# Performance work log

Hardware: AMD Instinct MI355X
Metric: run time of the kernel (lower is better)

## Reference

```python
import jax, jax.numpy as jnp
import numpy as np

B, N, DM, H = 2, 512, 1024, 16  # batch, seq, d_model, n_heads
DEPTHS = [1, 2, 4, 8]
LAM = 0.1  # lambda_distance


def setup_inputs() -> dict:
    key = jax.random.key(0)
    ks = jax.random.split(key, 2 + 5 * len(DEPTHS))
    inp = {
        "x": jax.random.normal(ks[0], (B, N, DM), jnp.float32),
        "depth_logits": jax.random.normal(ks[1], (len(DEPTHS),), jnp.float32),
    }
    j = 2
    for i, D in enumerate(DEPTHS):
        ds = DM // D
        r = max(1, D // 4)
        inp[f"pe{i}"] = jax.random.normal(ks[j], (N, D, ds), jnp.float32) * 0.02; j += 1
        inp[f"wqkv{i}"] = jax.random.normal(ks[j], (D, ds, 3 * ds), jnp.float32) / np.sqrt(ds); j += 1
        inp[f"wo{i}"] = jax.random.normal(ks[j], (DM, DM), jnp.float32) / np.sqrt(DM); j += 1
        inp[f"fu{i}"] = jax.random.normal(ks[j], (D, r), jnp.float32) / np.sqrt(r); j += 1
        inp[f"fv{i}"] = jax.random.normal(ks[j], (r, D), jnp.float32); j += 1
    return inp


def _ring_bias(n, lam, dtype):
    # toroidal (circular) distance bias on the sequence ring, normalized by N/2
    idx = jnp.arange(n)
    diff = jnp.abs(idx[:, None] - idx[None, :])
    ring = jnp.minimum(diff, n - diff).astype(dtype)
    return -lam * ring * (2.0 / n)  # [N, N]


def _toroidal_branch(x, pe, wqkv, wo, fu, fv):
    # x: [B, N, DM]; pe: [N, D, ds]; wqkv: [D, ds, 3ds]; wo: [DM, DM]; fu@fv: [D, D]
    b, n, dm = x.shape
    d_depth, ds, _ = wqkv.shape
    hd = ds // H
    xs = x.reshape(b, n, d_depth, ds) + pe[None]          # [B, N, D, ds]
    qkv = jnp.einsum('bnds,dse->bnde', xs, wqkv)          # per-depth-slice projection
    q, k, v = jnp.split(qkv, 3, axis=-1)
    q = q.reshape(b, n, d_depth, H, hd)
    k = k.reshape(b, n, d_depth, H, hd)
    v = v.reshape(b, n, d_depth, H, hd)
    bias = _ring_bias(n, LAM, x.dtype)
    scores = jnp.einsum('bndhe,bmdhe->bdhnm', q, k) / jnp.sqrt(jnp.asarray(hd, x.dtype))
    attn = jax.nn.softmax(scores + bias, axis=-1)          # [B, D, H, N, N]
    o = jnp.einsum('bdhnm,bmdhe->bndhe', attn, v).reshape(b, n, d_depth, ds)
    mix = fu @ fv                                          # low-rank depth fusion [D, D]
    fused = jnp.einsum('df,bnfs->bnds', mix, o).reshape(b, n, dm)
    return fused @ wo


def _forward(x, depth_logits, pe0, wqkv0, wo0, fu0, fv0, pe1, wqkv1, wo1, fu1, fv1,
             pe2, wqkv2, wo2, fu2, fv2, pe3, wqkv3, wo3, fu3, fv3):
    # inference-mode depth selection: hard one-hot at argmax (all branches still computed)
    w = jax.nn.one_hot(jnp.argmax(depth_logits), depth_logits.shape[0], dtype=x.dtype)
    params = [(pe0, wqkv0, wo0, fu0, fv0), (pe1, wqkv1, wo1, fu1, fv1),
              (pe2, wqkv2, wo2, fu2, fv2), (pe3, wqkv3, wo3, fu3, fv3)]
    out = jnp.zeros_like(x)
    for i, p in enumerate(params):
        out = out + w[i] * _toroidal_branch(x, *p)
    return out


def reference(x, depth_logits, pe0, wqkv0, wo0, fu0, fv0, pe1, wqkv1, wo1, fu1, fv1,
              pe2, wqkv2, wo2, fu2, fv2, pe3, wqkv3, wo3, fu3, fv3):
    return _forward(x, depth_logits, pe0, wqkv0, wo0, fu0, fv0, pe1, wqkv1, wo1, fu1, fv1,
                    pe2, wqkv2, wo2, fu2, fv2, pe3, wqkv3, wo3, fu3, fv3)
```

## Files before the change

### kernel.cpp

```cpp
#include <hip/hip_runtime.h>

#define B_   2
#define N_   512
#define DM_  1024
#define H_   16
#define LAM_ 0.1f

typedef __attribute__((ext_vector_type(8))) short bf16x8;
typedef __attribute__((ext_vector_type(4))) float f32x4;
typedef unsigned short ush;
struct ush4 { ush x, y, z, w; };
struct uint2s { unsigned x, y; };

__device__ inline ush f2bf(float v) {
    union { float f; unsigned u; } c; c.f = v;
    unsigned r = c.u + 0x7FFF + ((c.u >> 16) & 1);
    return (ush)(r >> 16);
}
__device__ inline float bf2f(ush b) {
    union { float f; unsigned u; } c; c.u = ((unsigned)b) << 16; return c.f;
}
__device__ inline f32x4 mfma16(bf16x8 a, bf16x8 b, f32x4 c) {
    return __builtin_amdgcn_mfma_f32_16x16x32_bf16(a, b, c, 0, 0, 0);
}

__global__ void k_select(const float* __restrict__ logits, int* __restrict__ sel) {
    if (threadIdx.x == 0) {
        float best = logits[0]; int bi = 0;
        for (int i = 1; i < 4; ++i) { float v = logits[i]; if (v > best) { best = v; bi = i; } }
        *sel = bi;
    }
}

template<int D>
__device__ void prep_wt_tile(int bT, int tid, const float* __restrict__ w,
                             ush* __restrict__ wh, ush* __restrict__ wl,
                             float (*lds)[65]) {
    constexpr int ds = DM_ / D;
    constexpr int tpr = 3 * ds / 64;
    constexpr int tpc = ds / 64;
    constexpr int tpd = tpr * tpc;
    if (bT >= D * tpd) return;
    const int d = bT / tpd, rem = bT % tpd;
    const int tr = rem / tpr, tc = rem % tpr;
    const float* src = w + (size_t)d * ds * 3 * ds;
    ush* dsth = wh + (size_t)d * 3 * ds * ds;
    ush* dstl = wl + (size_t)d * 3 * ds * ds;
    const int c = tid & 63, r0 = tid >> 6;
    #pragma unroll
    for (int j = 0; j < 16; ++j) {
        const int r = j * 4 + r0;
        lds[r][c] = src[(size_t)(tr * 64 + r) * (3 * ds) + tc * 64 + c];
    }
    __syncthreads();
    #pragma unroll
    for (int j = 0; j < 16; ++j) {
        const int r = j * 4 + r0;
        const float v = lds[c][r];
        const size_t o = (size_t)(tc * 64 + r) * ds + tr * 64 + c;
        const ush h = f2bf(v);
        dsth[o] = h; dstl[o] = f2bf(v - bf2f(h));
    }
}
__global__ __launch_bounds__(256) void k_prep(
        const int* __restrict__ sel, const float* __restrict__ x,
        const float* __restrict__ pe0, const float* __restrict__ pe1,
        const float* __restrict__ pe2, const float* __restrict__ pe3,
        const float* __restrict__ w0, const float* __restrict__ w1,
        const float* __restrict__ w2, const float* __restrict__ w3,
        const float* __restrict__ wo0, const float* __restrict__ wo1,
        const float* __restrict__ wo2, const float* __restrict__ wo3,
        ush* __restrict__ xh, ush* __restrict__ xl,
        ush* __restrict__ wqh, ush* __restrict__ wql,
        ush* __restrict__ woh, ush* __restrict__ wol) {
    __shared__ float lds[64][65];
    const int s = *sel;
    const int bid = blockIdx.x, tid = threadIdx.x;
    if (bid < 1024) {
        const float* pe = (s == 0) ? pe0 : (s == 1) ? pe1 : (s == 2) ? pe2 : pe3;
        const size_t i0 = ((size_t)bid * 256 + tid) * 4;
        const float4 xv = *(const float4*)&x[i0];
        const float4 pv = *(const float4*)&pe[i0 & ((size_t)N_ * DM_ - 1)];
        ush4 h4, l4;
        float v;
        v = xv.x + pv.x; h4.x = f2bf(v); l4.x = f2bf(v - bf2f(h4.x));
        v = xv.y + pv.y; h4.y = f2bf(v); l4.y = f2bf(v - bf2f(h4.y));
        v = xv.z + pv.z; h4.z = f2bf(v); l4.z = f2bf(v - bf2f(h4.z));
        v = xv.w + pv.w; h4.w = f2bf(v); l4.w = f2bf(v - bf2f(h4.w));
        *(ush4*)&xh[i0] = h4;
        *(ush4*)&xl[i0] = l4;
    } else if (bid < 1792) {
        const int bT = bid - 1024;
        switch (s) {
            case 0: prep_wt_tile<1>(bT, tid, w0, wqh, wql, lds); break;
            case 1: prep_wt_tile<2>(bT, tid, w1, wqh, wql, lds); break;
            case 2: prep_wt_tile<4>(bT, tid, w2, wqh, wql, lds); break;
            case 3: prep_wt_tile<8>(bT, tid, w3, wqh, wql, lds); break;
        }
    } else {
        const float* w = (s == 0) ? wo0 : (s == 1) ? wo1 : (s == 2) ? wo2 : wo3;
        const int bT = bid - 1792;
        const int tr = bT >> 4, tc = bT & 15;
        const int c = tid & 63, r0 = tid >> 6;
        #pragma unroll
        for (int j = 0; j < 16; ++j) {
            const int r = j * 4 + r0;
            lds[r][c] = w[(size_t)(tr * 64 + r) * DM_ + tc * 64 + c];
        }
        __syncthreads();
        #pragma unroll
        for (int j = 0; j < 16; ++j) {
            const int r = j * 4 + r0;
            const float v = lds[c][r];
            const size_t o = (size_t)(tc * 64 + r) * DM_ + tr * 64 + c;
            const ush h = f2bf(v);
            woh[o] = h; wol[o] = f2bf(v - bf2f(h));
        }
    }
}

template<int KD>
__device__ void gemm_core(const ush* __restrict__ Ah, const ush* __restrict__ Al, int lda,
                          const ush* __restrict__ Bh, const ush* __restrict__ Bl, int ldb,
                          int row0, int col0, int tid, ush* lds, f32x4 acc[2][2]) {
    ush* lAh = lds; ush* lAl = lds + 2560; ush* lBh = lds + 5120; ush* lBl = lds + 7680;
    const int srow = tid >> 2, scg = tid & 3;
    const int lane = tid & 63, w = tid >> 6;
    const int wm = w >> 1, wn = w & 1;
    const int lr = lane & 15, lb = lane >> 4;

    for (int k0 = 0; k0 < KD; k0 += 32) {
        *(bf16x8*)&lAh[srow * 40 + scg * 8] =
            *(const bf16x8*)&Ah[(size_t)(row0 + srow) * lda + k0 + scg * 8];
        *(bf16x8*)&lAl[srow * 40 + scg * 8] =
            *(const bf16x8*)&Al[(size_t)(row0 + srow) * lda + k0 + scg * 8];
        *(bf16x8*)&lBh[srow * 40 + scg * 8] =
            *(const bf16x8*)&Bh[(size_t)(col0 + srow) * ldb + k0 + scg * 8];
        *(bf16x8*)&lBl[srow * 40 + scg * 8] =
            *(const bf16x8*)&Bl[(size_t)(col0 + srow) * ldb + k0 + scg * 8];
        __syncthreads();
        bf16x8 ah[2], al[2], bh[2], bl[2];
        #pragma unroll
        for (int mg = 0; mg < 2; ++mg) {
            const int r = wm * 32 + mg * 16 + lr;
            ah[mg] = *(const bf16x8*)&lAh[r * 40 + lb * 8];
            al[mg] = *(const bf16x8*)&lAl[r * 40 + lb * 8];
        }
        #pragma unroll
        for (int ng = 0; ng < 2; ++ng) {
            const int r = wn * 32 + ng * 16 + lr;
            bh[ng] = *(const bf16x8*)&lBh[r * 40 + lb * 8];
            bl[ng] = *(const bf16x8*)&lBl[r * 40 + lb * 8];
        }
        #pragma unroll
        for (int mg = 0; mg < 2; ++mg)
            #pragma unroll
            for (int ng = 0; ng < 2; ++ng) {
                acc[mg][ng] = mfma16(ah[mg], bh[ng], acc[mg][ng]);
                acc[mg][ng] = mfma16(al[mg], bh[ng], acc[mg][ng]);
                acc[mg][ng] = mfma16(ah[mg], bl[ng], acc[mg][ng]);
            }
        __syncthreads();
    }
}

template<int D>
__device__ void qkv_body(int bid, int tid,
                         const ush* __restrict__ xh, const ush* __restrict__ xl,
                         const ush* __restrict__ wh, const ush* __restrict__ wl,
                         ush* __restrict__ Qh, ush* __restrict__ Ql,
                         ush* __restrict__ Kh, ush* __restrict__ Kl,
                         ush* __restrict__ Vth, ush* __restrict__ Vtl, ush* lds) {
    constexpr int ds = DM_ / D;
    constexpr int hd = ds / H_;
    constexpr int nx = 3 * ds / 64;
    const int bx = bid % nx, by = (bid / nx) & 7, bz = bid / (nx * 8);
    const int b = bz / D, d = bz % D;
    const int row0 = by * 64, col0 = bx * 64;

    f32x4 acc[2][2] = {};
    gemm_core<ds>(xh + (size_t)b * N_ * DM_ + d * ds, xl + (size_t)b * N_ * DM_ + d * ds, DM_,
                  wh + (size_t)d * 3 * ds * ds, wl + (size_t)d * 3 * ds * ds, ds,
                  row0, col0, tid, lds, acc);

    const int lane = tid & 63, w = tid >> 6;
    const int wm = w >> 1, wn = w & 1;
    const int lr = lane & 15, lb = lane >> 4;
    #pragma unroll
    for (int mg = 0; mg < 2; ++mg)
        #pragma unroll
        for (int ng = 0; ng < 2; ++ng) {
            const int n0 = row0 + wm * 32 + mg * 16 + lb * 4;
            const int e  = col0 + wn * 32 + ng * 16 + lr;
            const int part = e / ds, ep = e % ds;
            const int h = ep / hd, t = ep % hd;
            const size_t head = ((size_t)b * D + d) * H_ + h;
            if (part == 2) {
                ush4 h4, l4;
                const float v0 = acc[mg][ng][0], v1 = acc[mg][ng][1];
                const float v2 = acc[mg][ng][2], v3 = acc[mg][ng][3];
                h4.x = f2bf(v0); l4.x = f2bf(v0 - bf2f(h4.x));
                h4.y = f2bf(v1); l4.y = f2bf(v1 - bf2f(h4.y));
                h4.z = f2bf(v2); l4.z = f2bf(v2 - bf2f(h4.z));
                h4.w = f2bf(v3); l4.w = f2bf(v3 - bf2f(h4.w));
                const size_t o = (head * hd + t) * N_ + n0;
                *(ush4*)&Vth[o] = h4;
                *(ush4*)&Vtl[o] = l4;
            } else {
                #pragma unroll
                for (int i = 0; i < 4; ++i) {
                    const size_t o = (head * N_ + n0 + i) * hd + t;
                    const float v = acc[mg][ng][i];
                    const ush hh = f2bf(v), ll = f2bf(v - bf2f(hh));
                    if (part == 0) { Qh[o] = hh; Ql[o] = ll; }
                    else           { Kh[o] = hh; Kl[o] = ll; }
                }
            }
        }
}
__global__ __launch_bounds__(256) void k_qkv(
        const int* __restrict__ sel,
        const ush* __restrict__ xh, const ush* __restrict__ xl,
        const ush* __restrict__ wh, const ush* __restrict__ wl,
        ush* __restrict__ Qh, ush* __restrict__ Ql,
        ush* __restrict__ Kh, ush* __restrict__ Kl,
        ush* __restrict__ Vth, ush* __restrict__ Vtl) {
    __shared__ ush lds[4 * 2560];
    const int bid = blockIdx.x, tid = threadIdx.x;
    switch (*sel) {
        case 0: qkv_body<1>(bid, tid, xh, xl, wh, wl, Qh, Ql, Kh, Kl, Vth, Vtl, lds); break;
        case 1: qkv_body<2>(bid, tid, xh, xl, wh, wl, Qh, Ql, Kh, Kl, Vth, Vtl, lds); break;
        case 2: qkv_body<4>(bid, tid, xh, xl, wh, wl, Qh, Ql, Kh, Kl, Vth, Vtl, lds); break;
        case 3: qkv_body<8>(bid, tid, xh, xl, wh, wl, Qh, Ql, Kh, Kl, Vth, Vtl, lds); break;
    }
}

template<int D>
__device__ void attn_body(int bid, int tid,
        const ush* __restrict__ Qh, const ush* __restrict__ Ql,
        const ush* __restrict__ Kh, const ush* __restrict__ Kl,
        const ush* __restrict__ Vth, const ush* __restrict__ Vtl,
        float* __restrict__ O, ush* P, float* redl) {
    constexpr int ds = DM_ / D, hd = ds / H_;
    constexpr int CH = (hd >= 64) ? 2 : 1;
    constexpr int NT = (hd >= 16) ? hd / 16 : 1;
    constexpr int NHEAD = B_ * D * H_;
    constexpr int NB = NHEAD * 32;
    if (bid >= NB) return;
    const int bidr = (bid & 7) * (NB / 8) + (bid >> 3);
    const int head = bidr >> 5, qt = bidr & 31;
    const int h = head % H_, d = (head / H_) % D, b = head / (H_ * D);
    const int q0 = qt * 16;
    const size_t hb = (size_t)head * N_ * hd;
    const int lane = tid & 63, wk = tid >> 6;
    const int lr = lane & 15, lb = lane >> 4;
    const float L2E = 1.44269504f;
    const float SC  = rsqrtf((float)hd) * L2E;
    const float RB2 = LAM_ * (2.0f / N_) * L2E;
    const bf16x8 z8 = {0, 0, 0, 0, 0, 0, 0, 0};

    bf16x8 qah[CH], qal[CH];
    #pragma unroll
    for (int c = 0; c < CH; ++c) {
        const int k0 = c * 32 + lb * 8;
        bf16x8 vh = z8, vl = z8;
        if (k0 < hd) {
            const size_t o = hb + (size_t)(q0 + lr) * hd + k0;
            vh = *(const bf16x8*)&Qh[o];
            vl = *(const bf16x8*)&Ql[o];
        }
        qah[c] = vh; qal[c] = vl;
    }

    f32x4 s[8];
    #pragma unroll
    for (int t = 0; t < 8; ++t) {
        const int kj0 = wk * 128 + t * 16;
        f32x4 acc = {0.f, 0.f, 0.f, 0.f};
        #pragma unroll
        for (int c = 0; c < CH; ++c) {
            const int k0 = c * 32 + lb * 8;
            bf16x8 kh8 = z8, kl8 = z8;
            if (k0 < hd) {
                const size_t o = hb + (size_t)(kj0 + lr) * hd + k0;
                kh8 = *(const bf16x8*)&Kh[o];
                kl8 = *(const bf16x8*)&Kl[o];
            }
            acc = mfma16(kh8, qah[c], acc);
            acc = mfma16(kl8, qah[c], acc);
            acc = mfma16(kh8, qal[c], acc);
        }
        s[t] = acc;
    }

    ush* Pw = P + wk * 2048;
    const int q = q0 + lr;
    float ls = 0.f;
    #pragma unroll
    for (int t = 0; t < 8; ++t) {
        const int kbase = wk * 128 + t * 16 + lb * 4;
        float p[4];
        #pragma unroll
        for (int i = 0; i < 4; ++i) {
            int dd = q - (kbase + i); dd = dd < 0 ? -dd : dd;
            const int ring = (dd < N_ - dd) ? dd : (N_ - dd);
            p[i] = exp2f(s[t][i] * SC - RB2 * (float)ring);
        }
        unsigned pk0, pk1;
        asm("v_cvt_pk_bf16_f32 %0, %1, %2" : "=v"(pk0) : "v"(p[0]), "v"(p[1]));
        asm("v_cvt_pk_bf16_f32 %0, %1, %2" : "=v"(pk1) : "v"(p[2]), "v"(p[3]));
        union { unsigned u; float f; } c0, c1, c2, c3;
        c0.u = pk0 << 16; c1.u = pk0 & 0xffff0000u;
        c2.u = pk1 << 16; c3.u = pk1 & 0xffff0000u;
        ls += (c0.f + c1.f) + (c2.f + c3.f);
        const int off = ((lr << 8) + ((t * 16 + lb * 4) << 1)) ^ ((lr & 7) << 4);
        uint2s pv; pv.x = pk0; pv.y = pk1;
        *(uint2s*)((char*)Pw + off) = pv;
    }
    ls += __shfl_xor(ls, 16);
    ls += __shfl_xor(ls, 32);
    if (lb == 0) redl[wk * 16 + lr] = ls;

    f32x4 acc2[NT];
    #pragma unroll
    for (int tt = 0; tt < NT; ++tt) acc2[tt] = (f32x4){0.f, 0.f, 0.f, 0.f};
    #pragma unroll
    for (int jc = 0; jc < 4; ++jc) {
        int poff = ((lr << 8) + ((jc * 32 + lb * 8) << 1)) ^ ((lr & 7) << 4);
        const bf16x8 pa = *(const bf16x8*)((const char*)Pw + poff);
        #pragma unroll
        for (int tt = 0; tt < NT; ++tt) {
            const size_t o = hb + (size_t)(tt * 16 + lr) * N_ + wk * 128 + jc * 32 + lb * 8;
            const bf16x8 vh8 = *(const bf16x8*)&Vth[o];
            const bf16x8 vl8 = *(const bf16x8*)&Vtl[o];
            acc2[tt] = mfma16(pa, vh8, acc2[tt]);
            acc2[tt] = mfma16(pa, vl8, acc2[tt]);
        }
    }

    __syncthreads();
    float* res = (float*)P;
    if (wk != 0) {
        #pragma unroll
        for (int tt = 0; tt < NT; ++tt)
            #pragma unroll
            for (int i = 0; i < 4; ++i)
                res[((wk - 1) * NT + tt) * 256 + i * 64 + lane] = acc2[tt][i];
    }
    __syncthreads();
    if (wk == 0) {
        float linv[4];
        #pragma unroll
        for (int i = 0; i < 4; ++i) {
            const int r = lb * 4 + i;
            linv[i] = 1.0f / (redl[r] + redl[16 + r] + redl[32 + r] + redl[48 + r]);
        }
        #pragma unroll
        for (int tt = 0; tt < NT; ++tt)
            #pragma unroll
            for (int i = 0; i < 4; ++i) {
                const float o = acc2[tt][i]
                    + res[(0 * NT + tt) * 256 + i * 64 + lane]
                    + res[(1 * NT + tt) * 256 + i * 64 + lane]
                    + res[(2 * NT + tt) * 256 + i * 64 + lane];
                const int rn = q0 + lb * 4 + i;
                const int tc = tt * 16 + lr;
                if (tc < hd)
                    O[((size_t)b * N_ + rn) * DM_ + d * ds + h * hd + tc] = o * linv[i];
            }
    }
}
__global__ __launch_bounds__(256) void k_attn(
        const int* __restrict__ sel,
        const ush* __restrict__ Qh, const ush* __restrict__ Ql,
        const ush* __restrict__ Kh, const ush* __restrict__ Kl,
        const ush* __restrict__ Vth, const ush* __restrict__ Vtl,
        float* __restrict__ O) {
    __shared__ __align__(16) ush P[4 * 16 * 128];
    __shared__ float redl[64];
    const int bid = blockIdx.x, tid = threadIdx.x;
    switch (*sel) {
        case 0: attn_body<1>(bid, tid, Qh, Ql, Kh, Kl, Vth, Vtl, O, P, redl); break;
        case 1: attn_body<2>(bid, tid, Qh, Ql, Kh, Kl, Vth, Vtl, O, P, redl); break;
        case 2: attn_body<4>(bid, tid, Qh, Ql, Kh, Kl, Vth, Vtl, O, P, redl); break;
        case 3: attn_body<8>(bid, tid, Qh, Ql, Kh, Kl, Vth, Vtl, O, P, redl); break;
    }
}

template<int D>
__device__ void mix_body(int bid, int tid, const float* __restrict__ fu,
                         const float* __restrict__ fv, const float* __restrict__ O,
                         ush* __restrict__ Fh, ush* __restrict__ Fl, float* mixs) {
    constexpr int ds = DM_ / D;
    constexpr int R = (D / 4 > 0) ? (D / 4) : 1;
    if (tid < D * D) {
        const int d = tid / D, f = tid % D;
        float m = 0.f;
        #pragma unroll
        for (int rr = 0; rr < R; ++rr) m += fu[d * R + rr] * fv[rr * D + f];
        mixs[tid] = m;
    }
    __syncthreads();
    const size_t idx = (size_t)bid * 256 + tid;
    const int dm = (int)(idx % DM_);
    const size_t bn = idx / DM_;
    const int d = dm / ds, s0 = dm % ds;
    const float* Ob = O + bn * DM_ + s0;
    float acc = 0.f;
    #pragma unroll
    for (int f = 0; f < D; ++f) acc += mixs[d * D + f] * Ob[(size_t)f * ds];
    const ush hh = f2bf(acc);
    Fh[idx] = hh; Fl[idx] = f2bf(acc - bf2f(hh));
}
__global__ __launch_bounds__(256) void k_mix(
        const int* __restrict__ sel,
        const float* __restrict__ fu0, const float* __restrict__ fv0,
        const float* __restrict__ fu1, const float* __restrict__ fv1,
        const float* __restrict__ fu2, const float* __restrict__ fv2,
        const float* __restrict__ fu3, const float* __restrict__ fv3,
        const float* __restrict__ O, ush* __restrict__ Fh, ush* __restrict__ Fl) {
    __shared__ float mixs[64];
    const int bid = blockIdx.x, tid = threadIdx.x;
    switch (*sel) {
        case 0: mix_body<1>(bid, tid, fu0, fv0, O, Fh, Fl, mixs); break;
        case 1: mix_body<2>(bid, tid, fu1, fv1, O, Fh, Fl, mixs); break;
        case 2: mix_body<4>(bid, tid, fu2, fv2, O, Fh, Fl, mixs); break;
        case 3: mix_body<8>(bid, tid, fu3, fv3, O, Fh, Fl, mixs); break;
    }
}

__global__ __launch_bounds__(256) void k_wo(
        const ush* __restrict__ Fh, const ush* __restrict__ Fl,
        const ush* __restrict__ wh, const ush* __restrict__ wl,
        float* __restrict__ out) {
    __shared__ ush lA[2][32 * 40];
    __shared__ ush lB[2][64 * 40];
    const int tid = threadIdx.x;
    const int bx = blockIdx.x & 15, by = blockIdx.x >> 4;
    const int row0 = by * 32, col0 = bx * 64;
    const int lane = tid & 63, w = tid >> 6;
    const int wq = w >> 1, wn = w & 1;
    const int lr = lane & 15, lb = lane >> 4;
    f32x4 acc[2] = {};

    for (int k0 = 0; k0 < DM_; k0 += 32) {
        {
            const int half = tid >> 7, t2 = tid & 127;
            const int srow = t2 >> 2, scg = t2 & 3;
            const ush* src = half ? Fl : Fh;
            *(bf16x8*)&lA[half][srow * 40 + scg * 8] =
                *(const bf16x8*)&src[(size_t)(row0 + srow) * DM_ + k0 + scg * 8];
        }
        {
            const int srow = tid >> 2, scg = tid & 3;
            *(bf16x8*)&lB[0][srow * 40 + scg * 8] =
                *(const bf16x8*)&wh[(size_t)(col0 + srow) * DM_ + k0 + scg * 8];
            *(bf16x8*)&lB[1][srow * 40 + scg * 8] =
                *(const bf16x8*)&wl[(size_t)(col0 + srow) * DM_ + k0 + scg * 8];
        }
        __syncthreads();
        const int ar = wq * 16 + lr;
        const bf16x8 ah = *(const bf16x8*)&lA[0][ar * 40 + lb * 8];
        const bf16x8 al = *(const bf16x8*)&lA[1][ar * 40 + lb * 8];
        #pragma unroll
        for (int ng = 0; ng < 2; ++ng) {
            const int br = wn * 32 + ng * 16 + lr;
            const bf16x8 bh = *(const bf16x8*)&lB[0][br * 40 + lb * 8];
            const bf16x8 bl = *(const bf16x8*)&lB[1][br * 40 + lb * 8];
            acc[ng] = mfma16(ah, bh, acc[ng]);
            acc[ng] = mfma16(al, bh, acc[ng]);
            acc[ng] = mfma16(ah, bl, acc[ng]);
        }
        __syncthreads();
    }
    #pragma unroll
    for (int ng = 0; ng < 2; ++ng)
        #pragma unroll
        for (int i = 0; i < 4; ++i) {
            const int r = row0 + wq * 16 + lb * 4 + i;
            const int c = col0 + wn * 32 + ng * 16 + lr;
            out[(size_t)r * DM_ + c] = acc[ng][i];
        }
}

extern "C" void kernel_launch(void* const* d_in, const int* in_sizes, int n_in,
                              void* d_out, int out_size, void* d_ws, size_t ws_size,
                              hipStream_t stream) {
    const float* x      = (const float*)d_in[0];
    const float* logits = (const float*)d_in[1];
    float* out = (float*)d_out;

    char* p = (char*)d_ws;
    int* sel = (int*)p; p += 256;
    const size_t MB = 1024 * 1024;
    ush* Qh = (ush*)p; p += 2 * MB;
    ush* Ql = (ush*)p; p += 2 * MB;
    ush* Kh = (ush*)p; p += 2 * MB;
    ush* Kl = (ush*)p; p += 2 * MB;
    ush* Vth = (ush*)p; p += 2 * MB + 65536;
    ush* Vtl = (ush*)p; p += 2 * MB + 65536;
    float* O = (float*)p; p += 4 * MB;
    ush* xh = (ush*)p; p += 2 * MB;
    ush* xl = (ush*)p; p += 2 * MB;
    ush* wqh = (ush*)p; p += 6 * MB;
    ush* wql = (ush*)p; p += 6 * MB;
    ush* woh = (ush*)p; p += 2 * MB;
    ush* wol = (ush*)p; p += 2 * MB;
    ush* Fh = xh, *Fl = xl;

    k_select<<<1, 64, 0, stream>>>(logits, sel);
    k_prep<<<dim3(2048), dim3(256), 0, stream>>>(
        sel, x,
        (const float*)d_in[2], (const float*)d_in[7],
        (const float*)d_in[12], (const float*)d_in[17],
        (const float*)d_in[3], (const float*)d_in[8],
        (const float*)d_in[13], (const float*)d_in[18],
        (const float*)d_in[4], (const float*)d_in[9],
        (const float*)d_in[14], (const float*)d_in[19],
        xh, xl, wqh, wql, woh, wol);
    k_qkv<<<dim3(768), dim3(256), 0, stream>>>(sel, xh, xl, wqh, wql,
                                               Qh, Ql, Kh, Kl, Vth, Vtl);
    k_attn<<<dim3(8192), dim3(256), 0, stream>>>(sel, Qh, Ql, Kh, Kl, Vth, Vtl, O);
    k_mix<<<dim3(B_ * N_ * DM_ / 256), dim3(256), 0, stream>>>(
        sel,
        (const float*)d_in[5],  (const float*)d_in[6],
        (const float*)d_in[10], (const float*)d_in[11],
        (const float*)d_in[15], (const float*)d_in[16],
        (const float*)d_in[20], (const float*)d_in[21],
        O, Fh, Fl);
    k_wo<<<dim3(512), dim3(256), 0, stream>>>(Fh, Fl, woh, wol, out);
}
```

Baseline: 89.58 us.

## Use one wavefront per attention block, looping over key chunks

The attention kernel used four wavefronts per 16-query tile, each handling 128 keys, then combined partial outputs and row sums through LDS with two block barriers. Now a single 64-thread wavefront loops over all four 128-key chunks, accumulating P·V in registers. The row-sum reduction becomes wave shuffles, removing the cross-wave LDS reduction, the barriers and most of the shared memory. The trade-off is four times less parallelism per block, serialised chunk passes per wave, and reliance on more resident blocks per CU to hide latency.

```diff
diff --git a/kernel.cpp b/kernel.cpp
--- a/kernel.cpp
+++ b/kernel.cpp
@@ -240,20 +240,18 @@
         const ush* __restrict__ Qh, const ush* __restrict__ Ql,
         const ush* __restrict__ Kh, const ush* __restrict__ Kl,
         const ush* __restrict__ Vth, const ush* __restrict__ Vtl,
-        float* __restrict__ O, ush* P, float* redl) {
+        float* __restrict__ O, ush* P) {
     constexpr int ds = DM_ / D, hd = ds / H_;
     constexpr int CH = (hd >= 64) ? 2 : 1;
     constexpr int NT = (hd >= 16) ? hd / 16 : 1;
-    constexpr int NHEAD = B_ * D * H_;
-    constexpr int NB = NHEAD * 32;
+    constexpr int NB = B_ * D * H_ * 32;
     if (bid >= NB) return;
     const int bidr = (bid & 7) * (NB / 8) + (bid >> 3);
     const int head = bidr >> 5, qt = bidr & 31;
     const int h = head % H_, d = (head / H_) % D, b = head / (H_ * D);
     const int q0 = qt * 16;
     const size_t hb = (size_t)head * N_ * hd;
-    const int lane = tid & 63, wk = tid >> 6;
-    const int lr = lane & 15, lb = lane >> 4;
+    const int lr = tid & 15, lb = tid >> 4;
     const float L2E = 1.44269504f;
     const float SC  = rsqrtf((float)hd) * L2E;
     const float RB2 = LAM_ * (2.0f / N_) * L2E;
@@ -272,118 +270,102 @@
         qah[c] = vh; qal[c] = vl;
     }
 
-    f32x4 s[8];
-    #pragma unroll
-    for (int t = 0; t < 8; ++t) {
-        const int kj0 = wk * 128 + t * 16;
-        f32x4 acc = {0.f, 0.f, 0.f, 0.f};
-        #pragma unroll
-        for (int c = 0; c < CH; ++c) {
-            const int k0 = c * 32 + lb * 8;
-            bf16x8 kh8 = z8, kl8 = z8;
-            if (k0 < hd) {
-                const size_t o = hb + (size_t)(kj0 + lr) * hd + k0;
-                kh8 = *(const bf16x8*)&Kh[o];
-                kl8 = *(const bf16x8*)&Kl[o];
-            }
-            acc = mfma16(kh8, qah[c], acc);
-            acc = mfma16(kl8, qah[c], acc);
-            acc = mfma16(kh8, qal[c], acc);
-        }
-        s[t] = acc;
-    }
-
-    ush* Pw = P + wk * 2048;
     const int q = q0 + lr;
     float ls = 0.f;
-    #pragma unroll
-    for (int t = 0; t < 8; ++t) {
-        const int kbase = wk * 128 + t * 16 + lb * 4;
-        float p[4];
-        #pragma unroll
-        for (int i = 0; i < 4; ++i) {
-            int dd = q - (kbase + i); dd = dd < 0 ? -dd : dd;
-            const int ring = (dd < N_ - dd) ? dd : (N_ - dd);
-            p[i] = exp2f(s[t][i] * SC - RB2 * (float)ring);
-        }
-        unsigned pk0, pk1;
-        asm("v_cvt_pk_bf16_f32 %0, %1, %2" : "=v"(pk0) : "v"(p[0]), "v"(p[1]));
-        asm("v_cvt_pk_bf16_f32 %0, %1, %2" : "=v"(pk1) : "v"(p[2]), "v"(p[3]));
-        union { unsigned u; float f; } c0, c1, c2, c3;
-        c0.u = pk0 << 16; c1.u = pk0 & 0xffff0000u;
-        c2.u = pk1 << 16; c3.u = pk1 & 0xffff0000u;
-        ls += (c0.f + c1.f) + (c2.f + c3.f);
-        const int off = ((lr << 8) + ((t * 16 + lb * 4) << 1)) ^ ((lr & 7) << 4);
-        uint2s pv; pv.x = pk0; pv.y = pk1;
-        *(uint2s*)((char*)Pw + off) = pv;
-    }
+    f32x4 acc2[NT];
+    #pragma unroll
+    for (int tt = 0; tt < NT; ++tt) acc2[tt] = (f32x4){0.f, 0.f, 0.f, 0.f};
+
+    for (int pass = 0; pass < 4; ++pass) {
+        const int col0 = pass * 128;
+
+        f32x4 s[8];
+        #pragma unroll
+        for (int t = 0; t < 8; ++t) {
+            const int kj0 = col0 + t * 16;
+            f32x4 acc = {0.f, 0.f, 0.f, 0.f};
+            #pragma unroll
+            for (int c = 0; c < CH; ++c) {
+                const int k0 = c * 32 + lb * 8;
+                bf16x8 kh8 = z8, kl8 = z8;
+                if (k0 < hd) {
+                    const size_t o = hb + (size_t)(kj0 + lr) * hd + k0;
+                    kh8 = *(const bf16x8*)&Kh[o];
+                    kl8 = *(const bf16x8*)&Kl[o];
+                }
+                acc = mfma16(kh8, qah[c], acc);
+                acc = mfma16(kl8, qah[c], acc);
+                acc = mfma16(kh8, qal[c], acc);
+            }
+            s[t] = acc;
+        }
+
+        #pragma unroll
+        for (int t = 0; t < 8; ++t) {
+            const int kbase = col0 + t * 16 + lb * 4;
+            float p[4];
+            #pragma unroll
+            for (int i = 0; i < 4; ++i) {
+                int dd = q - (kbase + i); dd = dd < 0 ? -dd : dd;
+                const int ring = (dd < N_ - dd) ? dd : (N_ - dd);
+                p[i] = exp2f(s[t][i] * SC - RB2 * (float)ring);
+            }
+            unsigned pk0, pk1;
+            asm("v_cvt_pk_bf16_f32 %0, %1, %2" : "=v"(pk0) : "v"(p[0]), "v"(p[1]));
+            asm("v_cvt_pk_bf16_f32 %0, %1, %2" : "=v"(pk1) : "v"(p[2]), "v"(p[3]));
+            union { unsigned u; float f; } c0, c1, c2, c3;
+            c0.u = pk0 << 16; c1.u = pk0 & 0xffff0000u;
+            c2.u = pk1 << 16; c3.u = pk1 & 0xffff0000u;
+            ls += (c0.f + c1.f) + (c2.f + c3.f);
+            const int off = ((lr << 8) + ((t * 16 + lb * 4) << 1)) ^ ((lr & 7) << 4);
+            uint2s pv; pv.x = pk0; pv.y = pk1;
+            *(uint2s*)((char*)P + off) = pv;
+        }
+
+        #pragma unroll
+        for (int jc = 0; jc < 4; ++jc) {
+            int poff = ((lr << 8) + ((jc * 32 + lb * 8) << 1)) ^ ((lr & 7) << 4);
+            const bf16x8 pa = *(const bf16x8*)((const char*)P + poff);
+            #pragma unroll
+            for (int tt = 0; tt < NT; ++tt) {
+                const size_t o = hb + (size_t)(tt * 16 + lr) * N_ + col0 + jc * 32 + lb * 8;
+                const bf16x8 vh8 = *(const bf16x8*)&Vth[o];
+                const bf16x8 vl8 = *(const bf16x8*)&Vtl[o];
+                acc2[tt] = mfma16(pa, vh8, acc2[tt]);
+                acc2[tt] = mfma16(pa, vl8, acc2[tt]);
+            }
+        }
+    }
+
     ls += __shfl_xor(ls, 16);
     ls += __shfl_xor(ls, 32);
-    if (lb == 0) redl[wk * 16 + lr] = ls;
-
-    f32x4 acc2[NT];
-    #pragma unroll
-    for (int tt = 0; tt < NT; ++tt) acc2[tt] = (f32x4){0.f, 0.f, 0.f, 0.f};
-    #pragma unroll
-    for (int jc = 0; jc < 4; ++jc) {
-        int poff = ((lr << 8) + ((jc * 32 + lb * 8) << 1)) ^ ((lr & 7) << 4);
-        const bf16x8 pa = *(const bf16x8*)((const char*)Pw + poff);
-        #pragma unroll
-        for (int tt = 0; tt < NT; ++tt) {
-            const size_t o = hb + (size_t)(tt * 16 + lr) * N_ + wk * 128 + jc * 32 + lb * 8;
-            const bf16x8 vh8 = *(const bf16x8*)&Vth[o];
-            const bf16x8 vl8 = *(const bf16x8*)&Vtl[o];
-            acc2[tt] = mfma16(pa, vh8, acc2[tt]);
-            acc2[tt] = mfma16(pa, vl8, acc2[tt]);
-        }
-    }
-
-    __syncthreads();
-    float* res = (float*)P;
-    if (wk != 0) {
-        #pragma unroll
-        for (int tt = 0; tt < NT; ++tt)
-            #pragma unroll
-            for (int i = 0; i < 4; ++i)
-                res[((wk - 1) * NT + tt) * 256 + i * 64 + lane] = acc2[tt][i];
-    }
-    __syncthreads();
-    if (wk == 0) {
-        float linv[4];
+    float linv[4];
+    #pragma unroll
+    for (int i = 0; i < 4; ++i) linv[i] = 1.0f / __shfl(ls, lb * 4 + i);
+
+    #pragma unroll
+    for (int tt = 0; tt < NT; ++tt)
         #pragma unroll
         for (int i = 0; i < 4; ++i) {
-            const int r = lb * 4 + i;
-            linv[i] = 1.0f / (redl[r] + redl[16 + r] + redl[32 + r] + redl[48 + r]);
-        }
-        #pragma unroll
-        for (int tt = 0; tt < NT; ++tt)
-            #pragma unroll
-            for (int i = 0; i < 4; ++i) {
-                const float o = acc2[tt][i]
-                    + res[(0 * NT + tt) * 256 + i * 64 + lane]
-                    + res[(1 * NT + tt) * 256 + i * 64 + lane]
-                    + res[(2 * NT + tt) * 256 + i * 64 + lane];
-                const int rn = q0 + lb * 4 + i;
-                const int tc = tt * 16 + lr;
-                if (tc < hd)
-                    O[((size_t)b * N_ + rn) * DM_ + d * ds + h * hd + tc] = o * linv[i];
-            }
-    }
-}
-__global__ __launch_bounds__(256) void k_attn(
+            const int rn = q0 + lb * 4 + i;
+            const int tc = tt * 16 + lr;
+            if (tc < hd)
+                O[((size_t)b * N_ + rn) * DM_ + d * ds + h * hd + tc] = acc2[tt][i] * linv[i];
+        }
+}
+__global__ __launch_bounds__(64) void k_attn(
         const int* __restrict__ sel,
         const ush* __restrict__ Qh, const ush* __restrict__ Ql,
         const ush* __restrict__ Kh, const ush* __restrict__ Kl,
         const ush* __restrict__ Vth, const ush* __restrict__ Vtl,
         float* __restrict__ O) {
-    __shared__ __align__(16) ush P[4 * 16 * 128];
-    __shared__ float redl[64];
+    __shared__ __align__(16) ush P[16 * 128];
     const int bid = blockIdx.x, tid = threadIdx.x;
     switch (*sel) {
-        case 0: attn_body<1>(bid, tid, Qh, Ql, Kh, Kl, Vth, Vtl, O, P, redl); break;
-        case 1: attn_body<2>(bid, tid, Qh, Ql, Kh, Kl, Vth, Vtl, O, P, redl); break;
-        case 2: attn_body<4>(bid, tid, Qh, Ql, Kh, Kl, Vth, Vtl, O, P, redl); break;
-        case 3: attn_body<8>(bid, tid, Qh, Ql, Kh, Kl, Vth, Vtl, O, P, redl); break;
+        case 0: attn_body<1>(bid, tid, Qh, Ql, Kh, Kl, Vth, Vtl, O, P); break;
+        case 1: attn_body<2>(bid, tid, Qh, Ql, Kh, Kl, Vth, Vtl, O, P); break;
+        case 2: attn_body<4>(bid, tid, Qh, Ql, Kh, Kl, Vth, Vtl, O, P); break;
+        case 3: attn_body<8>(bid, tid, Qh, Ql, Kh, Kl, Vth, Vtl, O, P); break;
     }
 }
 
@@ -520,7 +502,7 @@
         xh, xl, wqh, wql, woh, wol);
     k_qkv<<<dim3(768), dim3(256), 0, stream>>>(sel, xh, xl, wqh, wql,
                                                Qh, Ql, Kh, Kl, Vth, Vtl);
-    k_attn<<<dim3(8192), dim3(256), 0, stream>>>(sel, Qh, Ql, Kh, Kl, Vth, Vtl, O);
+    k_attn<<<dim3(8192), dim3(64), 0, stream>>>(sel, Qh, Ql, Kh, Kl, Vth, Vtl, O);
     k_mix<<<dim3(B_ * N_ * DM_ / 256), dim3(256), 0, stream>>>(
         sel,
         (const float*)d_in[5],  (const float*)d_in[6],
```

Measured after the change: 95.97 us. 1.07x slower.
